# Kernel optimization log

Hardware: AMD Instinct MI355X
Metric: run time of the kernel (lower is better)

Reference implementation:

```python
import jax, jax.numpy as jnp
import numpy as np

B, L, H, C, K, S = 16, 336, 192, 862, 8, 8
FREQ = H // 2 + 1           # 97  (trunc_tail = 0)
NF = 2 * K + 1              # 17 filters per channel: [K lead | K diff | 1 self]
OUT_DIM = FREQ * NF         # 1649
MAX_SHIFT = 48


def setup_inputs() -> dict:
    key = jax.random.key(0)
    ks = jax.random.split(key, 14)
    sc = 0.02
    return {
        "x": jax.random.normal(ks[0], (B, L, C), jnp.float32),
        "y_hat": jax.random.normal(ks[1], (B, H, C), jnp.float32),
        "r_in": jax.random.uniform(ks[2], (B, C, K), jnp.float32, -1.0, 1.0),
        "temperature": jnp.ones((1,), jnp.float32),
        "classifier_w": jax.random.normal(ks[3], (S, L), jnp.float32) * sc,
        "basic_state": jax.random.normal(ks[4], (C, S), jnp.float32) * sc,
        "state_bias": jax.random.normal(ks[5], (S,), jnp.float32) * sc,
        "mix_head_w": jax.random.normal(ks[6], (S, K * OUT_DIM), jnp.float32) * sc,
        "mix_head_b": jax.random.normal(ks[7], (S, OUT_DIM), jnp.float32) * sc,
        "mix_w_real": jax.random.normal(ks[8], (FREQ, 3 * FREQ), jnp.float32) * sc,
        "mix_w_imag": jax.random.normal(ks[9], (FREQ, 3 * FREQ), jnp.float32) * sc,
        "mix_b_real": jax.random.normal(ks[10], (FREQ,), jnp.float32) * sc,
        "mix_b_imag": jax.random.normal(ks[11], (FREQ,), jnp.float32) * sc,
        "leader_ids": jax.random.randint(ks[12], (B, C, K), 0, C, jnp.int32),
        "shift": jax.random.randint(ks[13], (B, C, K), 0, MAX_SHIFT, jnp.int32),
    }


def reference(x, y_hat, r_in, temperature, classifier_w, basic_state, state_bias,
              mix_head_w, mix_head_b, mix_w_real, mix_w_imag, mix_b_real, mix_b_imag,
              leader_ids, shift):
    xt = jnp.transpose(x, (0, 2, 1))        # (B,C,L)
    yt = jnp.transpose(y_hat, (0, 2, 1))    # (B,C,H)
    # instance norm over time
    mu = xt.mean(-1, keepdims=True)
    xc = xt - mu
    std = jnp.sqrt((xc ** 2).mean(-1, keepdims=True) + 1e-8)
    xn = xc / std
    yn = (yt - mu) / std
    # ---- shifted_leader_seq (no-grad in torch) ----
    seq_all = jnp.concatenate([xn, yn], -1)                 # (B,C,L+H)
    b_idx = jnp.arange(B)[:, None, None]
    seq_leader = seq_all[b_idx, leader_ids]                 # (B,C,K,L+H)
    idx = jnp.arange(L, L + H, dtype=jnp.int32)[None, None, None, :] - shift[..., None]
    seq_shifted = jnp.take_along_axis(seq_leader, idx, axis=-1)   # (B,C,K,H)
    seq_shifted = jax.lax.stop_gradient(seq_shifted * jnp.sign(r_in)[..., None])
    r_abs = jax.lax.stop_gradient(jnp.abs(r_in))
    # softmax-weighted leader correlations (self channel weight = 1)
    ones = jnp.ones((B, C, 1), xn.dtype)
    r_soft = jax.nn.softmax(jnp.concatenate([ones, r_abs], -1) / temperature, axis=-1)  # (B,C,K+1)
    corr_feat = r_soft[..., 1:]                             # (B,C,K)
    # ---- FilterFactory: mixture-of-states dynamic filters ----
    p = jax.nn.softmax(state_bias + basic_state +
                       jnp.einsum('bcl,sl->bcs', xt, classifier_w), axis=-1)  # (B,C,S)
    weight = jnp.einsum('bcs,sf->bcf', p, mix_head_w).reshape(B, C, K, OUT_DIM)
    bias_o = jnp.einsum('bcs,so->bco', p, mix_head_b)       # (B,C,OUT_DIM)
    filt = (jnp.einsum('bck,bcko->bco', corr_feat, weight) + bias_o).reshape(B, C, NF, FREQ)
    # ---- FFT-domain fusion ----
    y_f = jnp.fft.rfft(yn)                                  # (B,C,FREQ) complex
    s_f = jnp.fft.rfft(seq_shifted)                         # (B,C,K,FREQ)
    diff_f = (s_f - y_f[:, :, None]) * filt[:, :, K:-1]
    lead_f = s_f * filt[:, :, :K]
    self_f = y_f * filt[:, :, -1]
    mix_in = jnp.concatenate([lead_f.sum(2), diff_f.sum(2), self_f], -1)  # (B,C,3*FREQ)
    w_c = mix_w_real + 1j * mix_w_imag
    b_c = mix_b_real + 1j * mix_b_imag
    mix_out = jnp.einsum('bcf,of->bco', mix_in, w_c) + b_c  # (B,C,FREQ)
    yn = yn + jnp.fft.irfft(mix_out, n=H)
    y_out = yn * std + mu
    return jnp.transpose(y_out, (0, 2, 1))                  # (B,H,C)
```

## Files before the change

kernel.cpp:

```cpp
#include <hip/hip_runtime.h>
#include <math.h>

#define BB 16
#define LL 336
#define HH 192
#define CC 862
#define KK 8
#define FREQ 97
#define OUTD 1649
#define OUTP 1664
#define TTOT 528
#define WINL 240
#define NBC (BB*CC)
#define PI_F 3.14159265358979323846f
#define WT 104
#define MIX_KS 19

typedef __attribute__((ext_vector_type(8))) short bf16x8;
typedef __attribute__((ext_vector_type(4))) float f32x4;

static __device__ __forceinline__ ushort f2bf(float f){
    unsigned u = __float_as_uint(f);
    unsigned r = (u + 0x7FFFu + ((u >> 16) & 1u)) >> 16;
    return (ushort)r;
}
static __device__ __forceinline__ float bf2f(ushort u){
    return __uint_as_float(((unsigned)u) << 16);
}

__global__ __launch_bounds__(256) void k_stats(
    const float* __restrict__ x, const float* __restrict__ r_in,
    const float* __restrict__ temp, const float* __restrict__ cw,
    const float* __restrict__ bstate, const float* __restrict__ sbias,
    float* __restrict__ w_mu, float* __restrict__ w_std, float* __restrict__ w_istd,
    float* __restrict__ w_sgn, float* __restrict__ w_A)
{
    __shared__ float red[4][64][10];
    int tid = threadIdx.x;
    int lane = tid & 63, q = tid >> 6;
    int bc = blockIdx.x*64 + lane;
    int b = bc / CC, c = bc - b*CC;
    float sum = 0.f, sq = 0.f, lg[8];
#pragma unroll
    for (int s=0;s<8;++s) lg[s]=0.f;
    if (bc < NBC){
        const float* xp = x + (size_t)b*LL*CC + c;
        int l0 = q*84;
        for (int l = l0; l < l0+84; ++l){
            float v = xp[(size_t)l*CC];
            sum += v; sq += v*v;
#pragma unroll
            for (int s=0;s<8;++s) lg[s] = fmaf(v, cw[s*LL+l], lg[s]);
        }
    }
    red[q][lane][0] = sum; red[q][lane][1] = sq;
#pragma unroll
    for (int s=0;s<8;++s) red[q][lane][2+s] = lg[s];
    __syncthreads();
    if (tid < 64 && bc < NBC){
        sum = 0.f; sq = 0.f;
#pragma unroll
        for (int s=0;s<8;++s) lg[s] = 0.f;
#pragma unroll
        for (int qq=0;qq<4;++qq){
            sum += red[qq][lane][0]; sq += red[qq][lane][1];
#pragma unroll
            for (int s=0;s<8;++s) lg[s] += red[qq][lane][2+s];
        }
        float mu   = sum * (1.f/LL);
        float var  = sq * (1.f/LL) - mu*mu;
        float stdv = sqrtf(var + 1e-8f);
        float istd = 1.f/stdv;
#pragma unroll
        for (int s=0;s<8;++s) lg[s] += sbias[s] + bstate[c*8+s];
        float m = lg[0];
#pragma unroll
        for (int s=1;s<8;++s) m = fmaxf(m, lg[s]);
        float p[8]; float den = 0.f;
#pragma unroll
        for (int s=0;s<8;++s){ p[s] = expf(lg[s]-m); den += p[s]; }
        float iden = 1.f/den;
#pragma unroll
        for (int s=0;s<8;++s) p[s] *= iden;

        float invT = 1.f / temp[0];
        float ek[8], sg[8];
        float dsum = expf(invT);
#pragma unroll
        for (int k=0;k<8;++k){
            float r = r_in[(size_t)bc*8 + k];
            sg[k] = (r > 0.f) ? 1.f : ((r < 0.f) ? -1.f : 0.f);
            ek[k] = expf(fabsf(r)*invT);
            dsum += ek[k];
        }
        float idsum = 1.f/dsum;

        w_mu[bc] = mu; w_std[bc] = stdv; w_istd[bc] = istd;
#pragma unroll
        for (int k=0;k<8;++k) w_sgn[(size_t)bc*8+k] = sg[k];
        float* Ar = w_A + (size_t)bc*80;
#pragma unroll
        for (int s=0;s<8;++s)
#pragma unroll
            for (int k=0;k<8;++k) Ar[s*8+k] = p[s]*(ek[k]*idsum);
#pragma unroll
        for (int s=0;s<8;++s) Ar[64+s] = p[s];
    }
}

__global__ __launch_bounds__(256) void k_win(
    const float* __restrict__ x, const float* __restrict__ y,
    const float* __restrict__ w_mu, const float* __restrict__ w_istd,
    float* __restrict__ win)
{
    __shared__ float buf[32][33];
    int b  = blockIdx.x;
    int t0 = blockIdx.y*32;
    int c0 = blockIdx.z*32;
    int tx = threadIdx.x, ty = threadIdx.y;
#pragma unroll
    for (int i=0;i<4;++i){
        int tl = ty + i*8;
        int t  = 289 + t0 + tl;
        int c  = c0 + tx;
        float v = 0.f;
        if (t < TTOT && c < CC){
            float raw = (t < LL) ? x[((size_t)b*LL + t)*CC + c]
                                 : y[((size_t)b*HH + (t-LL))*CC + c];
            int bc = b*CC + c;
            v = (raw - w_mu[bc]) * w_istd[bc];
        }
        buf[tl][tx] = v;
    }
    __syncthreads();
#pragma unroll
    for (int i=0;i<4;++i){
        int cl = ty + i*8;
        int c  = c0 + cl;
        int wl = t0 + tx;
        if (wl < 239 && c < CC)
            win[(size_t)(b*CC + c)*WINL + wl] = buf[tx][cl];
    }
}

__global__ __launch_bounds__(640) void k_pq(
    const float* __restrict__ wr, const float* __restrict__ wi,
    const float* __restrict__ br, const float* __restrict__ bi,
    float* __restrict__ PQ, float* __restrict__ cst)
{
    int h = blockIdx.x;
    int tid = threadIdx.x;
    __shared__ float a_s[97], b_s[97], t_s[97];
    if (tid < 97){
        int o = tid;
        int mmod = (o*h) % 192;
        float th = (2.f*PI_F/192.f) * (float)mmod;
        float sn, cs; sincosf(th, &sn, &cs);
        float aa, bb;
        if (o == 0)      { aa = 1.f/192.f;                      bb = 0.f; }
        else if (o == 96){ aa = ((h&1)? -1.f:1.f)/192.f;        bb = 0.f; }
        else             { aa = 2.f*cs/192.f;                   bb = -2.f*sn/192.f; }
        a_s[o]=aa; b_s[o]=bb;
        t_s[o] = aa*br[o] + bb*bi[o];
    }
    __syncthreads();
    if (tid < 582){
        int j = tid;
        int isP = (j < 291);
        int jj = isP ? j : j-291;
        float acc = 0.f;
        for (int o=0;o<97;++o){
            float wrv = wr[o*291+jj], wiv = wi[o*291+jj];
            acc += isP ? (a_s[o]*wrv + b_s[o]*wiv)
                       : (b_s[o]*wrv - a_s[o]*wiv);
        }
        PQ[(size_t)j*HH + h] = acc;
    }
    if (tid == 0){
        float s = 0.f;
        for (int o=0;o<97;++o) s += t_s[o];
        cst[h] = s;
    }
}

__global__ __launch_bounds__(256) void k_bfrag(ushort* __restrict__ bfrag)
{
    int idx = blockIdx.x*256 + threadIdx.x;
    const int total = 13*3*64*8;
    if (idx >= total) return;
    int j  = idx & 7;
    int l  = (idx >> 3) & 63;
    int tk = idx >> 9;
    int t  = tk / 3, kk = tk - t*3;
    int k  = kk*32 + ((l>>4)<<3) + j;
    int nl = l & 15;
    float v = 0.f;
    if (t < 7){
        int n = t*16 + nl;
        if (n < 98){
            int g  = n >> 1;
            int mm = (g*k) % 96;
            float th = (2.f*PI_F/96.f)*(float)mm;
            float sn, cs; sincosf(th, &sn, &cs);
            v = (n & 1) ? -sn : cs;
        }
    } else {
        int n = (t-7)*16 + nl;
        int f = n | 1;
        int mm = (f*k) % 192;
        float th = (2.f*PI_F/192.f)*(float)mm;
        float sn, cs; sincosf(th, &sn, &cs);
        v = (n & 1) ? -sn : cs;
    }
    bfrag[idx] = f2bf(v);
}

__global__ __launch_bounds__(256) void k_wpack(
    const float* __restrict__ mhw, const float* __restrict__ mhb,
    ushort* __restrict__ wfrag)
{
    int idx = blockIdx.x*256 + threadIdx.x;
    const int total = WT*3*64*8;
    if (idx >= total) return;
    int j  = idx & 7;
    int l  = (idx >> 3) & 63;
    int tk = idx >> 9;
    int t  = tk / 3, kk = tk - t*3;
    int k  = kk*32 + ((l>>4)<<3) + j;
    int n  = t*16 + (l & 15);
    float v = 0.f;
    if (n < OUTD && k < 80){
        v = (k < 64) ? mhw[(size_t)(k>>3)*(8*OUTD) + (size_t)(k&7)*OUTD + n]
                     : mhb[(size_t)(k-64)*OUTD + n];
    }
    wfrag[idx] = f2bf(v);
}

__global__ __launch_bounds__(256) void k_pqpack(
    const float* __restrict__ PQ, ushort* __restrict__ pqfrag)
{
    int idx = blockIdx.x*256 + threadIdx.x;
    const int total = 12*MIX_KS*64*8;
    if (idx >= total) return;
    int j  = idx & 7;
    int l  = (idx >> 3) & 63;
    int tk = idx >> 9;
    int t  = tk / MIX_KS, kk = tk - t*MIX_KS;
    int k  = kk*32 + ((l>>4)<<3) + j;
    int n  = t*16 + (l & 15);
    float v = (k < 582) ? PQ[(size_t)k*HH + n] : 0.f;
    pqfrag[idx] = f2bf(v);
}

__global__ __launch_bounds__(256) void k_filt(
    const float* __restrict__ A, const ushort* __restrict__ wfrag,
    ushort* __restrict__ filt)
{
    __shared__ __align__(16) ushort Abf[16*104];
    int tid = threadIdx.x;
    int bc0 = blockIdx.x*16;
    for (int i = tid; i < 16*96; i += 256){
        int r = i/96, j = i - r*96;
        float v = (j < 80) ? A[(size_t)(bc0+r)*80 + j] : 0.f;
        Abf[r*104 + j] = f2bf(v);
    }
    __syncthreads();
    int wid = tid >> 6, lane = tid & 63;
    int lrow = lane & 15, lk8 = (lane >> 4) << 3, row0 = (lane >> 4)*4;
    bf16x8 a0 = *(const bf16x8*)&Abf[lrow*104 +  0 + lk8];
    bf16x8 a1 = *(const bf16x8*)&Abf[lrow*104 + 32 + lk8];
    bf16x8 a2 = *(const bf16x8*)&Abf[lrow*104 + 64 + lk8];
    for (int t = wid*26; t < wid*26 + 26; ++t){
        const ushort* wb = wfrag + (size_t)(t*3)*512 + lane*8;
        f32x4 acc = {0.f,0.f,0.f,0.f};
        acc = __builtin_amdgcn_mfma_f32_16x16x32_bf16(a0, *(const bf16x8*)(wb       ), acc, 0,0,0);
        acc = __builtin_amdgcn_mfma_f32_16x16x32_bf16(a1, *(const bf16x8*)(wb +  512), acc, 0,0,0);
        acc = __builtin_amdgcn_mfma_f32_16x16x32_bf16(a2, *(const bf16x8*)(wb + 1024), acc, 0,0,0);
        int n = t*16 + lrow;
        if (n < OUTD){
#pragma unroll
            for (int r = 0; r < 4; ++r)
                filt[(size_t)(bc0+row0+r)*OUTP + n] = f2bf(acc[r]);
        }
    }
}

__global__ __launch_bounds__(256) void k_dft(
    const float* __restrict__ win, const ushort* __restrict__ filtb,
    const float* __restrict__ w_sgn, const int* __restrict__ leader,
    const int* __restrict__ shiftp, const ushort* __restrict__ bfrag,
    ushort* __restrict__ mixin)
{
    __shared__ __align__(16) ushort Ae[16*104];
    __shared__ __align__(16) ushort Ao[16*104];
    __shared__ float sfl[2][9][97];
    __shared__ __align__(4) ushort flu[OUTP];
    __shared__ int   rbase[9];
    __shared__ float rsgn[9];
    int bc = blockIdx.x;
    int tid = threadIdx.x;
    int b = bc / CC, c = bc - b*CC;
    if (tid < 9){
        int k = tid;
        int src_c = c, sh = 0; float sg = 1.f;
        if (k < 8){
            src_c = leader[(size_t)bc*8 + k];
            sh    = shiftp[(size_t)bc*8 + k];
            sg    = w_sgn[(size_t)bc*8 + k];
        }
        rbase[k] = (b*CC + src_c)*WINL + 47 - sh;
        rsgn[k]  = sg;
    }
    for (int i = tid; i < OUTP/2; i += 256)
        *(unsigned*)&flu[i*2] = *(const unsigned*)&filtb[(size_t)bc*OUTP + i*2];
    __syncthreads();
    for (int i = tid; i < 864; i += 256){
        int r = i/96, hh = i - r*96;
        const float* wp = win + (size_t)rbase[r];
        float sg = rsgn[r];
        float x0 = wp[hh]*sg, x1 = wp[hh+96]*sg;
        Ae[r*104+hh] = f2bf(x0 + x1);
        Ao[r*104+hh] = f2bf(x0 - x1);
    }
    __syncthreads();
    int wid = tid >> 6, lane = tid & 63;
    int lrow = lane & 15;
    int lk8  = (lane >> 4) << 3;
    int row0 = (lane >> 4) * 4;
    for (int t = wid; t < 13; t += 4){
        const ushort* Ab = (t < 7) ? Ae : Ao;
        const ushort* bb = bfrag + (size_t)(t*3)*512 + lane*8;
        f32x4 acc = {0.f, 0.f, 0.f, 0.f};
#pragma unroll
        for (int kk = 0; kk < 3; ++kk){
            bf16x8 a = *(const bf16x8*)&Ab[lrow*104 + kk*32 + lk8];
            acc = __builtin_amdgcn_mfma_f32_16x16x32_bf16(a, *(const bf16x8*)(bb + kk*512), acc, 0, 0, 0);
        }
#pragma unroll
        for (int r = 0; r < 4; ++r){
            int row = row0 + r;
            if (row <= 8){
                if (t < 7){
                    int n = t*16 + lrow;
                    if (n < 98) sfl[n & 1][row][n & ~1] = acc[r];
                } else {
                    int n = (t-7)*16 + lrow;
                    sfl[n & 1][row][n | 1] = acc[r];
                }
            }
        }
    }
    __syncthreads();
    if (tid < 194){
        int p = (tid >= 97) ? 1 : 0;
        int fr = tid - 97*p;
        float yv = sfl[p][8][fr];
        float ls = 0.f, ds = 0.f;
#pragma unroll
        for (int k=0;k<8;++k){
            float sv = sfl[p][k][fr];
            float f1 = bf2f(flu[k*FREQ+fr]), f2 = bf2f(flu[(8+k)*FREQ+fr]);
            ls = fmaf(sv, f1, ls);
            ds = fmaf(sv - yv, f2, ds);
        }
        float f3 = bf2f(flu[16*FREQ+fr]);
        ushort* mrow = mixin + (size_t)bc*582 + p*291;
        mrow[fr]       = f2bf(ls);
        mrow[97 + fr]  = f2bf(ds);
        mrow[194 + fr] = f2bf(yv*f3);
    }
}

__global__ __launch_bounds__(256) void k_mix(
    const ushort* __restrict__ mixin, const ushort* __restrict__ pqfrag,
    const float* __restrict__ cst, const float* __restrict__ win,
    const float* __restrict__ w_mu, const float* __restrict__ w_std,
    float* __restrict__ out)
{
    __shared__ __align__(16) ushort Abf[16*616];
    int tid = threadIdx.x;
    int bc0 = blockIdx.x*16;
    for (int i = tid; i < 16*304; i += 256){
        int r = i/304, jc = i - r*304;
        unsigned v = 0u;
        if (jc < 291) v = *(const unsigned*)&mixin[(size_t)(bc0+r)*582 + jc*2];
        *(unsigned*)&Abf[r*616 + jc*2] = v;
    }
    __syncthreads();
    int wid = tid >> 6, lane = tid & 63;
    int lrow = lane & 15, lk8 = (lane >> 4) << 3, row0 = (lane >> 4)*4;
    f32x4 acc0 = {0.f,0.f,0.f,0.f}, acc1 = {0.f,0.f,0.f,0.f}, acc2 = {0.f,0.f,0.f,0.f};
    const ushort* pq0 = pqfrag + (size_t)((wid*3+0)*MIX_KS)*512 + lane*8;
    const ushort* pq1 = pqfrag + (size_t)((wid*3+1)*MIX_KS)*512 + lane*8;
    const ushort* pq2 = pqfrag + (size_t)((wid*3+2)*MIX_KS)*512 + lane*8;
    for (int kk = 0; kk < MIX_KS; ++kk){
        bf16x8 a = *(const bf16x8*)&Abf[lrow*616 + kk*32 + lk8];
        acc0 = __builtin_amdgcn_mfma_f32_16x16x32_bf16(a, *(const bf16x8*)(pq0 + (size_t)kk*512), acc0, 0,0,0);
        acc1 = __builtin_amdgcn_mfma_f32_16x16x32_bf16(a, *(const bf16x8*)(pq1 + (size_t)kk*512), acc1, 0,0,0);
        acc2 = __builtin_amdgcn_mfma_f32_16x16x32_bf16(a, *(const bf16x8*)(pq2 + (size_t)kk*512), acc2, 0,0,0);
    }
#pragma unroll
    for (int tl = 0; tl < 3; ++tl){
        f32x4 acc = (tl==0) ? acc0 : ((tl==1) ? acc1 : acc2);
        int h = (wid*3 + tl)*16 + lrow;
        float cs = cst[h];
#pragma unroll
        for (int r = 0; r < 4; ++r){
            int bc = bc0 + row0 + r;
            int b = bc / CC, c = bc - b*CC;
            float yn = win[(size_t)bc*WINL + 47 + h];
            float v = (acc[r] + cs + yn)*w_std[bc] + w_mu[bc];
            out[((size_t)b*HH + h)*CC + c] = v;
        }
    }
}

extern "C" void kernel_launch(void* const* d_in, const int* in_sizes, int n_in,
                              void* d_out, int out_size, void* d_ws, size_t ws_size,
                              hipStream_t stream) {
    const float* x      = (const float*)d_in[0];
    const float* y      = (const float*)d_in[1];
    const float* r_in   = (const float*)d_in[2];
    const float* temp   = (const float*)d_in[3];
    const float* cw     = (const float*)d_in[4];
    const float* bstate = (const float*)d_in[5];
    const float* sbias  = (const float*)d_in[6];
    const float* mhw    = (const float*)d_in[7];
    const float* mhb    = (const float*)d_in[8];
    const float* wr     = (const float*)d_in[9];
    const float* wi     = (const float*)d_in[10];
    const float* br     = (const float*)d_in[11];
    const float* bi     = (const float*)d_in[12];
    const int*   leader = (const int*)d_in[13];
    const int*   shiftp = (const int*)d_in[14];
    float* ws  = (float*)d_ws;
    float* out = (float*)d_out;

    size_t o_win  = 0;
    size_t o_mu   = o_win  + (size_t)NBC*WINL;
    size_t o_std  = o_mu   + NBC;
    size_t o_istd = o_std  + NBC;
    size_t o_sgn  = o_istd + NBC;
    size_t o_A    = o_sgn  + (size_t)NBC*8;
    size_t o_filt = o_A    + (size_t)NBC*80;
    size_t o_mix  = o_filt + (size_t)NBC*OUTP/2;
    size_t o_PQ   = o_mix  + (size_t)NBC*291;
    size_t o_cst  = o_PQ   + (size_t)582*HH;
    size_t o_bfr  = o_cst  + HH;
    size_t o_wfr  = o_bfr  + 19968/2;
    size_t o_pqf  = o_wfr  + 159744/2;

    ushort* filtb  = (ushort*)(ws + o_filt);
    ushort* mixinb = (ushort*)(ws + o_mix);
    ushort* bfrag  = (ushort*)(ws + o_bfr);
    ushort* wfrag  = (ushort*)(ws + o_wfr);
    ushort* pqfrag = (ushort*)(ws + o_pqf);

    k_stats<<<dim3((NBC+63)/64), dim3(256), 0, stream>>>(
        x, r_in, temp, cw, bstate, sbias,
        ws+o_mu, ws+o_std, ws+o_istd, ws+o_sgn, ws+o_A);

    k_win<<<dim3(BB, 8, 27), dim3(32, 8), 0, stream>>>(
        x, y, ws+o_mu, ws+o_istd, ws+o_win);

    k_pq<<<dim3(HH), dim3(640), 0, stream>>>(
        wr, wi, br, bi, ws+o_PQ, ws+o_cst);

    k_bfrag<<<dim3(78), dim3(256), 0, stream>>>(bfrag);
    k_wpack<<<dim3((WT*3*64*8+255)/256), dim3(256), 0, stream>>>(mhw, mhb, wfrag);
    k_pqpack<<<dim3((12*MIX_KS*64*8+255)/256), dim3(256), 0, stream>>>(ws+o_PQ, pqfrag);

    k_filt<<<dim3(NBC/16), dim3(256), 0, stream>>>(ws+o_A, wfrag, filtb);

    k_dft<<<dim3(NBC), dim3(256), 0, stream>>>(
        ws+o_win, filtb, ws+o_sgn, leader, shiftp, bfrag, mixinb);

    k_mix<<<dim3(NBC/16), dim3(256), 0, stream>>>(
        mixinb, pqfrag, ws+o_cst, ws+o_win, ws+o_mu, ws+o_std, out);
}
```

Before: 249.4 us.

## Merge pack kernels, widen stats block, and trim LDS staging in DFT kernel

Combines the three weight/twiddle packing kernels into one launch to cut launch overhead. Doubles k_stats threads to 512 so each thread reduces half as many time steps, raising parallelism on the strided column reads. In k_dft, drops the shared-memory copy of the filter row and reads filter values directly from global memory, and packs the even/odd DFT input as bf16 pairs to halve the LDS stores. The direct global filter reads trade LDS traffic for uncoalesced-ish global loads, and the sfl row is padded to 104.

```diff
diff --git a/kernel.cpp b/kernel.cpp
--- a/kernel.cpp
+++ b/kernel.cpp
@@ -1,4 +1,5 @@
 #include <hip/hip_runtime.h>
+#include <hip/hip_bf16.h>
 #include <math.h>
 
 #define BB 16
@@ -15,6 +16,7 @@
 #define PI_F 3.14159265358979323846f
 #define WT 104
 #define MIX_KS 19
+#define SFP 104
 
 typedef __attribute__((ext_vector_type(8))) short bf16x8;
 typedef __attribute__((ext_vector_type(4))) float f32x4;
@@ -28,14 +30,14 @@
     return __uint_as_float(((unsigned)u) << 16);
 }
 
-__global__ __launch_bounds__(256) void k_stats(
+__global__ __launch_bounds__(512) void k_stats(
     const float* __restrict__ x, const float* __restrict__ r_in,
     const float* __restrict__ temp, const float* __restrict__ cw,
     const float* __restrict__ bstate, const float* __restrict__ sbias,
     float* __restrict__ w_mu, float* __restrict__ w_std, float* __restrict__ w_istd,
     float* __restrict__ w_sgn, float* __restrict__ w_A)
 {
-    __shared__ float red[4][64][10];
+    __shared__ float red[8][64][10];
     int tid = threadIdx.x;
     int lane = tid & 63, q = tid >> 6;
     int bc = blockIdx.x*64 + lane;
@@ -45,8 +47,8 @@
     for (int s=0;s<8;++s) lg[s]=0.f;
     if (bc < NBC){
         const float* xp = x + (size_t)b*LL*CC + c;
-        int l0 = q*84;
-        for (int l = l0; l < l0+84; ++l){
+        int l0 = q*42;
+        for (int l = l0; l < l0+42; ++l){
             float v = xp[(size_t)l*CC];
             sum += v; sq += v*v;
 #pragma unroll
@@ -62,7 +64,7 @@
 #pragma unroll
         for (int s=0;s<8;++s) lg[s] = 0.f;
 #pragma unroll
-        for (int qq=0;qq<4;++qq){
+        for (int qq=0;qq<8;++qq){
             sum += red[qq][lane][0]; sq += red[qq][lane][1];
 #pragma unroll
             for (int s=0;s<8;++s) lg[s] += red[qq][lane][2+s];
@@ -183,73 +185,67 @@
     }
 }
 
-__global__ __launch_bounds__(256) void k_bfrag(ushort* __restrict__ bfrag)
-{
-    int idx = blockIdx.x*256 + threadIdx.x;
-    const int total = 13*3*64*8;
-    if (idx >= total) return;
-    int j  = idx & 7;
-    int l  = (idx >> 3) & 63;
-    int tk = idx >> 9;
-    int t  = tk / 3, kk = tk - t*3;
-    int k  = kk*32 + ((l>>4)<<3) + j;
-    int nl = l & 15;
-    float v = 0.f;
-    if (t < 7){
-        int n = t*16 + nl;
-        if (n < 98){
-            int g  = n >> 1;
-            int mm = (g*k) % 96;
-            float th = (2.f*PI_F/96.f)*(float)mm;
+#define NBFR (13*3*64*8)
+#define NWFR (WT*3*64*8)
+#define NPQF (12*MIX_KS*64*8)
+__global__ __launch_bounds__(256) void k_pack(
+    const float* __restrict__ mhw, const float* __restrict__ mhb,
+    const float* __restrict__ PQ,
+    ushort* __restrict__ bfrag, ushort* __restrict__ wfrag, ushort* __restrict__ pqfrag)
+{
+    int gidx = blockIdx.x*256 + threadIdx.x;
+    if (gidx < NBFR){
+        int idx = gidx;
+        int j  = idx & 7;
+        int l  = (idx >> 3) & 63;
+        int tk = idx >> 9;
+        int t  = tk / 3, kk = tk - t*3;
+        int k  = kk*32 + ((l>>4)<<3) + j;
+        int nl = l & 15;
+        float v = 0.f;
+        if (t < 7){
+            int n = t*16 + nl;
+            if (n < 98){
+                int g  = n >> 1;
+                int mm = (g*k) % 96;
+                float th = (2.f*PI_F/96.f)*(float)mm;
+                float sn, cs; sincosf(th, &sn, &cs);
+                v = (n & 1) ? -sn : cs;
+            }
+        } else {
+            int n = (t-7)*16 + nl;
+            int f = n | 1;
+            int mm = (f*k) % 192;
+            float th = (2.f*PI_F/192.f)*(float)mm;
             float sn, cs; sincosf(th, &sn, &cs);
             v = (n & 1) ? -sn : cs;
         }
-    } else {
-        int n = (t-7)*16 + nl;
-        int f = n | 1;
-        int mm = (f*k) % 192;
-        float th = (2.f*PI_F/192.f)*(float)mm;
-        float sn, cs; sincosf(th, &sn, &cs);
-        v = (n & 1) ? -sn : cs;
-    }
-    bfrag[idx] = f2bf(v);
-}
-
-__global__ __launch_bounds__(256) void k_wpack(
-    const float* __restrict__ mhw, const float* __restrict__ mhb,
-    ushort* __restrict__ wfrag)
-{
-    int idx = blockIdx.x*256 + threadIdx.x;
-    const int total = WT*3*64*8;
-    if (idx >= total) return;
-    int j  = idx & 7;
-    int l  = (idx >> 3) & 63;
-    int tk = idx >> 9;
-    int t  = tk / 3, kk = tk - t*3;
-    int k  = kk*32 + ((l>>4)<<3) + j;
-    int n  = t*16 + (l & 15);
-    float v = 0.f;
-    if (n < OUTD && k < 80){
-        v = (k < 64) ? mhw[(size_t)(k>>3)*(8*OUTD) + (size_t)(k&7)*OUTD + n]
-                     : mhb[(size_t)(k-64)*OUTD + n];
-    }
-    wfrag[idx] = f2bf(v);
-}
-
-__global__ __launch_bounds__(256) void k_pqpack(
-    const float* __restrict__ PQ, ushort* __restrict__ pqfrag)
-{
-    int idx = blockIdx.x*256 + threadIdx.x;
-    const int total = 12*MIX_KS*64*8;
-    if (idx >= total) return;
-    int j  = idx & 7;
-    int l  = (idx >> 3) & 63;
-    int tk = idx >> 9;
-    int t  = tk / MIX_KS, kk = tk - t*MIX_KS;
-    int k  = kk*32 + ((l>>4)<<3) + j;
-    int n  = t*16 + (l & 15);
-    float v = (k < 582) ? PQ[(size_t)k*HH + n] : 0.f;
-    pqfrag[idx] = f2bf(v);
+        bfrag[idx] = f2bf(v);
+    } else if (gidx < NBFR + NWFR){
+        int idx = gidx - NBFR;
+        int j  = idx & 7;
+        int l  = (idx >> 3) & 63;
+        int tk = idx >> 9;
+        int t  = tk / 3, kk = tk - t*3;
+        int k  = kk*32 + ((l>>4)<<3) + j;
+        int n  = t*16 + (l & 15);
+        float v = 0.f;
+        if (n < OUTD && k < 80){
+            v = (k < 64) ? mhw[(size_t)(k>>3)*(8*OUTD) + (size_t)(k&7)*OUTD + n]
+                         : mhb[(size_t)(k-64)*OUTD + n];
+        }
+        wfrag[idx] = f2bf(v);
+    } else if (gidx < NBFR + NWFR + NPQF){
+        int idx = gidx - NBFR - NWFR;
+        int j  = idx & 7;
+        int l  = (idx >> 3) & 63;
+        int tk = idx >> 9;
+        int t  = tk / MIX_KS, kk = tk - t*MIX_KS;
+        int k  = kk*32 + ((l>>4)<<3) + j;
+        int n  = t*16 + (l & 15);
+        float v = (k < 582) ? PQ[(size_t)k*HH + n] : 0.f;
+        pqfrag[idx] = f2bf(v);
+    }
 }
 
 __global__ __launch_bounds__(256) void k_filt(
@@ -293,8 +289,7 @@
 {
     __shared__ __align__(16) ushort Ae[16*104];
     __shared__ __align__(16) ushort Ao[16*104];
-    __shared__ float sfl[2][9][97];
-    __shared__ __align__(4) ushort flu[OUTP];
+    __shared__ float sfl[2][9][SFP];
     __shared__ int   rbase[9];
     __shared__ float rsgn[9];
     int bc = blockIdx.x;
@@ -311,16 +306,18 @@
         rbase[k] = (b*CC + src_c)*WINL + 47 - sh;
         rsgn[k]  = sg;
     }
-    for (int i = tid; i < OUTP/2; i += 256)
-        *(unsigned*)&flu[i*2] = *(const unsigned*)&filtb[(size_t)bc*OUTP + i*2];
-    __syncthreads();
-    for (int i = tid; i < 864; i += 256){
-        int r = i/96, hh = i - r*96;
+    __syncthreads();
+    for (int u = tid; u < 432; u += 256){
+        int r = u/48, jj = u - r*48;
+        int hh = 2*jj;
         const float* wp = win + (size_t)rbase[r];
         float sg = rsgn[r];
-        float x0 = wp[hh]*sg, x1 = wp[hh+96]*sg;
-        Ae[r*104+hh] = f2bf(x0 + x1);
-        Ao[r*104+hh] = f2bf(x0 - x1);
+        float x00 = wp[hh]*sg,    x01 = wp[hh+1]*sg;
+        float x10 = wp[hh+96]*sg, x11 = wp[hh+97]*sg;
+        __hip_bfloat162 se = __float22bfloat162_rn(float2{x00+x10, x01+x11});
+        __hip_bfloat162 so = __float22bfloat162_rn(float2{x00-x10, x01-x11});
+        *(__hip_bfloat162*)&Ae[r*104+hh] = se;
+        *(__hip_bfloat162*)&Ao[r*104+hh] = so;
     }
     __syncthreads();
     int wid = tid >> 6, lane = tid & 63;
@@ -354,16 +351,17 @@
     if (tid < 194){
         int p = (tid >= 97) ? 1 : 0;
         int fr = tid - 97*p;
+        const ushort* fb = filtb + (size_t)bc*OUTP + fr;
         float yv = sfl[p][8][fr];
         float ls = 0.f, ds = 0.f;
 #pragma unroll
         for (int k=0;k<8;++k){
             float sv = sfl[p][k][fr];
-            float f1 = bf2f(flu[k*FREQ+fr]), f2 = bf2f(flu[(8+k)*FREQ+fr]);
+            float f1 = bf2f(fb[k*FREQ]), f2 = bf2f(fb[(8+k)*FREQ]);
             ls = fmaf(sv, f1, ls);
             ds = fmaf(sv - yv, f2, ds);
         }
-        float f3 = bf2f(flu[16*FREQ+fr]);
+        float f3 = bf2f(fb[16*FREQ]);
         ushort* mrow = mixin + (size_t)bc*582 + p*291;
         mrow[fr]       = f2bf(ls);
         mrow[97 + fr]  = f2bf(ds);
@@ -447,8 +445,8 @@
     size_t o_PQ   = o_mix  + (size_t)NBC*291;
     size_t o_cst  = o_PQ   + (size_t)582*HH;
     size_t o_bfr  = o_cst  + HH;
-    size_t o_wfr  = o_bfr  + 19968/2;
-    size_t o_pqf  = o_wfr  + 159744/2;
+    size_t o_wfr  = o_bfr  + NBFR/2;
+    size_t o_pqf  = o_wfr  + NWFR/2;
 
     ushort* filtb  = (ushort*)(ws + o_filt);
     ushort* mixinb = (ushort*)(ws + o_mix);
@@ -456,7 +454,7 @@
     ushort* wfrag  = (ushort*)(ws + o_wfr);
     ushort* pqfrag = (ushort*)(ws + o_pqf);
 
-    k_stats<<<dim3((NBC+63)/64), dim3(256), 0, stream>>>(
+    k_stats<<<dim3((NBC+63)/64), dim3(512), 0, stream>>>(
         x, r_in, temp, cw, bstate, sbias,
         ws+o_mu, ws+o_std, ws+o_istd, ws+o_sgn, ws+o_A);
 
@@ -466,9 +464,8 @@
     k_pq<<<dim3(HH), dim3(640), 0, stream>>>(
         wr, wi, br, bi, ws+o_PQ, ws+o_cst);
 
-    k_bfrag<<<dim3(78), dim3(256), 0, stream>>>(bfrag);
-    k_wpack<<<dim3((WT*3*64*8+255)/256), dim3(256), 0, stream>>>(mhw, mhb, wfrag);
-    k_pqpack<<<dim3((12*MIX_KS*64*8+255)/256), dim3(256), 0, stream>>>(ws+o_PQ, pqfrag);
+    k_pack<<<dim3((NBFR+NWFR+NPQF+255)/256), dim3(256), 0, stream>>>(
+        mhw, mhb, ws+o_PQ, bfrag, wfrag, pqfrag);
 
     k_filt<<<dim3(NBC/16), dim3(256), 0, stream>>>(ws+o_A, wfrag, filtb);
 
```

After: 229.7 us. -7.9%, faster.
